# Kernel optimization log

Hardware: AMD Instinct MI355X
Metric: run time of the kernel (lower is better)

The kernel has to match this reference:

```python
import jax, jax.numpy as jnp
import numpy as np

N_NODES = 100000
N_EDGES = 300000
N_GRAPHS = 4096
EMB = 256
L = 5
EPS = 1e-5


def setup_inputs() -> dict:
    key = jax.random.key(0)
    ks = jax.random.split(key, 16)
    x = jax.random.normal(ks[0], (N_NODES, 40), dtype=jnp.float32)
    edge_index = jax.random.randint(ks[1], (2, N_EDGES), 0, N_NODES, dtype=jnp.int32)
    edge_attr = jax.random.normal(ks[2], (N_EDGES, 10), dtype=jnp.float32)
    batch = jnp.sort(jax.random.randint(ks[3], (N_NODES,), 0, N_GRAPHS, dtype=jnp.int32))
    s = lambda fan: 1.0 / np.sqrt(fan)
    params = {
        "x_emb_W": jax.random.normal(ks[4], (EMB, 40), jnp.float32) * np.sqrt(2.0 / 40),
        "x_emb_b": jnp.zeros((EMB,), jnp.float32),
        "e_emb_W": jax.random.normal(ks[5], (EMB, 10), jnp.float32) * np.sqrt(2.0 / 10),
        "e_emb_b": jnp.zeros((EMB,), jnp.float32),
        "gcn_W": jax.random.normal(ks[6], (L, EMB, EMB), jnp.float32) * s(EMB),
        "gcn_b": jax.random.normal(ks[7], (L, EMB), jnp.float32) * s(EMB),
        "root_emb": jax.random.normal(ks[8], (L, EMB), jnp.float32),
        "bn_gamma": jnp.ones((L, EMB), jnp.float32),
        "bn_beta": jnp.zeros((L, EMB), jnp.float32),
        "p1_W": jax.random.normal(ks[9], (EMB // 2, EMB), jnp.float32) * s(EMB),
        "p1_b": jnp.zeros((EMB // 2,), jnp.float32),
        "p2_W": jax.random.normal(ks[10], (EMB // 2, EMB // 2), jnp.float32) * s(EMB // 2),
        "p2_b": jnp.zeros((EMB // 2,), jnp.float32),
        "p3_W": jax.random.normal(ks[11], (1, EMB // 2), jnp.float32) * s(EMB // 2),
        "p3_b": jnp.zeros((1,), jnp.float32),
    }
    return dict(x=x, edge_index=edge_index, edge_attr=edge_attr, batch=batch, **params)


def _gcn_conv(h, row, col, ea, W, b, root):
    # h: [N, D] node feats; ea: [E, D] edge feats
    hx = h @ W.T + b
    deg = jax.ops.segment_sum(jnp.ones_like(row, dtype=hx.dtype), row, num_segments=N_NODES) + 1.0
    dinv = deg ** -0.5
    norm = dinv[row] * dinv[col]                      # [E]
    msg = norm[:, None] * jax.nn.relu(hx[row] + ea)   # gather + relu + scale
    agg = jax.ops.segment_sum(msg, col, num_segments=N_NODES)  # scatter-add to targets
    return agg + jax.nn.relu(hx + root) / deg[:, None]


def _batchnorm(h, gamma, beta):
    mean = jnp.mean(h, axis=0)
    var = jnp.var(h, axis=0)
    return (h - mean) * jax.lax.rsqrt(var + EPS) * gamma + beta


def reference(x, edge_index, edge_attr, batch,
              x_emb_W, x_emb_b, e_emb_W, e_emb_b,
              gcn_W, gcn_b, root_emb, bn_gamma, bn_beta,
              p1_W, p1_b, p2_W, p2_b, p3_W, p3_b):
    row, col = edge_index[0], edge_index[1]
    h = x @ x_emb_W.T + x_emb_b
    ea = edge_attr @ e_emb_W.T + e_emb_b
    for l in range(L):
        h_in = h
        h = _gcn_conv(h, row, col, ea, gcn_W[l], gcn_b[l], root_emb[l])
        h = _batchnorm(h_in + h, bn_gamma[l], bn_beta[l])
        if l != L - 1:
            h = jax.nn.relu(h)
        # dropout is identity in eval mode
    # global mean pool over graphs
    sums = jax.ops.segment_sum(h, batch, num_segments=N_GRAPHS)
    cnts = jax.ops.segment_sum(jnp.ones((h.shape[0],), h.dtype), batch, num_segments=N_GRAPHS)
    g = sums / jnp.maximum(cnts, 1.0)[:, None]
    # prediction head: Lin-ReLU-Lin-ReLU-Lin
    g = jax.nn.relu(g @ p1_W.T + p1_b)
    g = jax.nn.relu(g @ p2_W.T + p2_b)
    return g @ p3_W.T + p3_b
```

## Files before the change

### kernel.cpp

```cpp
#include <hip/hip_runtime.h>
#include <hip/hip_bf16.h>

#define NN 100000
#define NE 300000
#define NG 4096
#define EMB 256
#define NLAYERS 5

typedef unsigned short u16;
typedef unsigned int u32;

typedef short bf16x8 __attribute__((ext_vector_type(8)));
typedef float f32x4 __attribute__((ext_vector_type(4)));

__device__ __forceinline__ float b2f(u16 u){
    union { float f; u32 i; } v; v.i = ((u32)u) << 16; return v.f;
}
__device__ __forceinline__ u16 f2b(float f){
    __hip_bfloat16 h = __float2bfloat16(f);
    union { __hip_bfloat16 h; u16 u; } v; v.h = h; return v.u;
}

#define XNB 32
__global__ __launch_bounds__(256) void embed_x(const float* __restrict__ x,
        const float* __restrict__ W, const float* __restrict__ b,
        u16* __restrict__ t)
{
    __shared__ float sW[256][41];
    __shared__ float sx[XNB][40];
    int tid = threadIdx.x;
    for (int i = tid; i < 256*40; i += 256) sW[i/40][i%40] = W[i];
    int n0 = blockIdx.x * XNB;
    for (int i = tid; i < XNB*40; i += 256) {
        int j = i/40, k = i%40;
        sx[j][k] = x[(size_t)(n0+j)*40 + k];
    }
    __syncthreads();
    float bb = b[tid];
    for (int j = 0; j < XNB; ++j) {
        float a = bb;
        #pragma unroll
        for (int k = 0; k < 40; ++k) a = fmaf(sW[tid][k], sx[j][k], a);
        t[(size_t)(n0+j)*EMB + tid] = f2b(a);
    }
}

__global__ void wconv(const float* __restrict__ W, u16* __restrict__ Wb, int n)
{
    int i = blockIdx.x*256 + threadIdx.x;
    if (i < n) Wb[i] = f2b(W[i]);
}

__global__ void ewt_kernel(const float* __restrict__ eW, float* __restrict__ eWt)
{
    int i = blockIdx.x*256 + threadIdx.x;
    if (i < 2560) { int f = i/10, k = i%10; eWt[k*256 + f] = eW[i]; }
}

__global__ void hist_kernel(const int* __restrict__ row, const int* __restrict__ col,
        int* __restrict__ rcnt, int* __restrict__ ccnt, int E)
{
    int e = blockIdx.x*256 + threadIdx.x;
    if (e < E) {
        atomicAdd(&rcnt[row[e]], 1);
        atomicAdd(&ccnt[col[e]], 1);
    }
}

__global__ void deg_fin(const int* __restrict__ rcnt, float* __restrict__ dinv,
                        float* __restrict__ invdg, int N)
{
    int n = blockIdx.x*256 + threadIdx.x;
    if (n < N) {
        float d = (float)rcnt[n] + 1.0f;
        dinv[n]  = rsqrtf(d);
        invdg[n] = 1.0f/d;
    }
}

__global__ void scan1(const int* __restrict__ cnt, int* __restrict__ bsum, int N)
{
    __shared__ int sh[256];
    int t = threadIdx.x, i = blockIdx.x*256 + t;
    sh[t] = (i < N) ? cnt[i] : 0;
    __syncthreads();
    for (int off = 128; off > 0; off >>= 1) {
        if (t < off) sh[t] += sh[t+off];
        __syncthreads();
    }
    if (t == 0) bsum[blockIdx.x] = sh[0];
}

__global__ __launch_bounds__(512) void scan2(const int* __restrict__ bsum,
        int* __restrict__ bbase, int* __restrict__ coff, int nb)
{
    __shared__ int a[512], b[512];
    int t = threadIdx.x;
    a[t] = (t < nb) ? bsum[t] : 0;
    __syncthreads();
    int* src = a; int* dst = b;
    for (int off = 1; off < 512; off <<= 1) {
        dst[t] = (t >= off) ? src[t-off] + src[t] : src[t];
        __syncthreads();
        int* tmp = src; src = dst; dst = tmp;
    }
    bbase[t] = t ? src[t-1] : 0;
    if (t == 0) coff[NN] = NE;
}

__global__ void scan3(const int* __restrict__ cnt, const int* __restrict__ bbase,
        int* __restrict__ coff, int N)
{
    __shared__ int a[256], b[256];
    int t = threadIdx.x, i = blockIdx.x*256 + t;
    a[t] = (i < N) ? cnt[i] : 0;
    __syncthreads();
    int* src = a; int* dst = b;
    for (int off = 1; off < 256; off <<= 1) {
        dst[t] = (t >= off) ? src[t-off] + src[t] : src[t];
        __syncthreads();
        int* tmp = src; src = dst; dst = tmp;
    }
    if (i < N) coff[i] = bbase[blockIdx.x] + (t ? src[t-1] : 0);
}

__global__ void csr_fill(const int* __restrict__ row, const int* __restrict__ col,
        const float* __restrict__ eattr, const int* __restrict__ coff,
        const float* __restrict__ dinv, int* __restrict__ fill,
        int* __restrict__ erow, float* __restrict__ enorm,
        u16* __restrict__ eab, int E)
{
    int e = blockIdx.x*256 + threadIdx.x;
    if (e < E) {
        int c = col[e], r = row[e];
        int p = coff[c] + atomicAdd(&fill[c], 1);
        erow[p]  = r;
        enorm[p] = dinv[r] * dinv[c];
        #pragma unroll
        for (int k = 0; k < 10; ++k) eab[(size_t)p*16 + k] = f2b(eattr[(size_t)e*10 + k]);
        #pragma unroll
        for (int k = 10; k < 16; ++k) eab[(size_t)p*16 + k] = 0;
    }
}

#define BM 128
#define BK 64
__global__ __launch_bounds__(256) void gemm_mfma(const u16* __restrict__ A,
        const u16* __restrict__ Wb, const float* __restrict__ bias,
        const float* __restrict__ bnsc, int doBN,
        u16* __restrict__ C, int M)
{
    __shared__ u16 As[BM*BK];
    __shared__ u16 Bs[BM*BK];
    __shared__ float scS[256], shS[256];
    const int tid  = threadIdx.x;
    if (doBN) { scS[tid] = bnsc[tid]; shS[tid] = bnsc[256+tid]; }
    const int wid  = tid >> 6;
    const int lane = tid & 63;
    const int wr = wid >> 1, wc = wid & 1;
    const int m0 = blockIdx.x * BM;
    const int n0 = blockIdx.y * BM;
    __syncthreads();
    f32x4 acc[4][4] = {};
    for (int k0 = 0; k0 < 256; k0 += BK) {
        #pragma unroll
        for (int i = 0; i < 4; ++i) {
            int L = tid + i*256;
            int rowi = L >> 3, ch = L & 7;
            int sw = ch ^ (rowi & 7);
            int gr = m0 + rowi; gr = gr < M ? gr : M-1;
            uint4 va = *reinterpret_cast<const uint4*>(&A[(size_t)gr*256 + k0 + ch*8]);
            if (doBN) {
                int kk = k0 + ch*8;
                u32 wv[4] = {va.x, va.y, va.z, va.w};
                #pragma unroll
                for (int j = 0; j < 4; ++j) {
                    float lo = b2f((u16)(wv[j] & 0xffffu));
                    float hi = b2f((u16)(wv[j] >> 16));
                    lo = fmaxf(fmaf(lo, scS[kk+2*j],   shS[kk+2*j]),   0.f);
                    hi = fmaxf(fmaf(hi, scS[kk+2*j+1], shS[kk+2*j+1]), 0.f);
                    wv[j] = (u32)f2b(lo) | ((u32)f2b(hi) << 16);
                }
                va.x = wv[0]; va.y = wv[1]; va.z = wv[2]; va.w = wv[3];
            }
            *reinterpret_cast<uint4*>(&As[(rowi*8 + sw)*8]) = va;
            uint4 vb = *reinterpret_cast<const uint4*>(&Wb[(size_t)(n0+rowi)*256 + k0 + ch*8]);
            *reinterpret_cast<uint4*>(&Bs[(rowi*8 + sw)*8]) = vb;
        }
        __syncthreads();
        const int c = lane >> 4;
        const int rl = lane & 15;
        #pragma unroll
        for (int kt = 0; kt < 2; ++kt) {
            bf16x8 af[4], bfr[4];
            #pragma unroll
            for (int f = 0; f < 4; ++f) {
                int ra = wr*64 + f*16 + rl;
                int cha = (kt*4 + c) ^ (ra & 7);
                af[f] = *reinterpret_cast<const bf16x8*>(&As[(ra*8 + cha)*8]);
                int rb = wc*64 + f*16 + rl;
                int chb = (kt*4 + c) ^ (rb & 7);
                bfr[f] = *reinterpret_cast<const bf16x8*>(&Bs[(rb*8 + chb)*8]);
            }
            #pragma unroll
            for (int fm = 0; fm < 4; ++fm)
                #pragma unroll
                for (int fn = 0; fn < 4; ++fn)
                    acc[fm][fn] = __builtin_amdgcn_mfma_f32_16x16x32_bf16(
                        af[fm], bfr[fn], acc[fm][fn], 0, 0, 0);
        }
        __syncthreads();
    }
    const int cn = lane & 15, rq = lane >> 4;
    #pragma unroll
    for (int fn = 0; fn < 4; ++fn) {
        int n = n0 + wc*64 + fn*16 + cn;
        float bb = bias[n];
        #pragma unroll
        for (int fm = 0; fm < 4; ++fm) {
            #pragma unroll
            for (int r = 0; r < 4; ++r) {
                int m = m0 + wr*64 + fm*16 + rq*4 + r;
                if (m < M) C[(size_t)m*256 + n] = f2b(acc[fm][fn][r] + bb);
            }
        }
    }
}

#define GFB 4
#define NGROUPS (NN/GFB)
__global__ __launch_bounds__(256) void gather_combine(const int* __restrict__ erow,
        const float* __restrict__ enorm, const u16* __restrict__ eab,
        const int* __restrict__ coff,
        const float* __restrict__ eWt, const float* __restrict__ ebv,
        const u16* __restrict__ hx, const float* __restrict__ rootv,
        const float* __restrict__ invdg, const float* __restrict__ bnscPrev,
        int doBN, u16* __restrict__ t, float* __restrict__ stats, int N)
{
    __shared__ float red[4][512];
    const int wid = threadIdx.x >> 6, lane = threadIdx.x & 63;
    const int f4 = lane*4;
    float w[4][10], bb[4];
    #pragma unroll
    for (int k = 0; k < 10; ++k) {
        float4 wv = *reinterpret_cast<const float4*>(&eWt[k*256 + f4]);
        w[0][k] = wv.x; w[1][k] = wv.y; w[2][k] = wv.z; w[3][k] = wv.w;
    }
    { float4 bv = *reinterpret_cast<const float4*>(&ebv[f4]);
      bb[0]=bv.x; bb[1]=bv.y; bb[2]=bv.z; bb[3]=bv.w; }
    float4 root = *reinterpret_cast<const float4*>(&rootv[f4]);
    float sc[4] = {1,1,1,1}, sh[4] = {0,0,0,0};
    if (doBN) {
        float4 s = *reinterpret_cast<const float4*>(&bnscPrev[f4]);
        float4 b = *reinterpret_cast<const float4*>(&bnscPrev[256+f4]);
        sc[0]=s.x; sc[1]=s.y; sc[2]=s.z; sc[3]=s.w;
        sh[0]=b.x; sh[1]=b.y; sh[2]=b.z; sh[3]=b.w;
    }
    float sacc[4] = {0,0,0,0}, s2acc[4] = {0,0,0,0};

    for (int g = blockIdx.x*4 + wid; g < NGROUPS; g += gridDim.x*4) {
        const int nb = g*GFB;
        int c1 = coff[nb+1], c2 = coff[nb+2], c3 = coff[nb+3], c4 = coff[nb+4];
        int s = coff[nb], e = c4;
        int jn = 0, cend = c1;
        float acc[4] = {0,0,0,0};

        #define FLUSH() do {                                                   \
            int n_ = nb + jn;                                                  \
            size_t idx_ = (size_t)n_*EMB + f4;                                 \
            uint2 hv_ = *reinterpret_cast<const uint2*>(&t[idx_]);             \
            uint2 xv_ = *reinterpret_cast<const uint2*>(&hx[idx_]);            \
            float id_ = invdg[n_];                                             \
            float hh_[4] = { b2f((u16)(hv_.x&0xffffu)), b2f((u16)(hv_.x>>16)), \
                             b2f((u16)(hv_.y&0xffffu)), b2f((u16)(hv_.y>>16)) };\
            float xx_[4] = { b2f((u16)(xv_.x&0xffffu)), b2f((u16)(xv_.x>>16)), \
                             b2f((u16)(xv_.y&0xffffu)), b2f((u16)(xv_.y>>16)) };\
            float rt_[4] = { root.x, root.y, root.z, root.w };                 \
            u16 ov_[4];                                                        \
            _Pragma("unroll")                                                  \
            for (int jj = 0; jj < 4; ++jj) {                                   \
                float hin_ = hh_[jj];                                          \
                if (doBN) hin_ = fmaxf(fmaf(hin_, sc[jj], sh[jj]), 0.f);       \
                float rv_ = xx_[jj] + rt_[jj];                                 \
                rv_ = rv_ > 0.f ? rv_ : 0.f;                                   \
                float tv_ = hin_ + acc[jj] + rv_*id_;                          \
                ov_[jj] = f2b(tv_);                                            \
                sacc[jj] += tv_; s2acc[jj] += tv_*tv_;                         \
                acc[jj] = 0.f;                                                 \
            }                                                                  \
            uint2 o_; o_.x = (u32)ov_[0] | ((u32)ov_[1]<<16);                  \
            o_.y = (u32)ov_[2] | ((u32)ov_[3]<<16);                            \
            *reinterpret_cast<uint2*>(&t[idx_]) = o_;                          \
            ++jn; cend = (jn==1) ? c2 : (jn==2) ? c3 : c4;                     \
        } while(0)

        #define CONSUME(nm, hvv, alo, ahi) do {                                \
            float hf_[4] = { b2f((u16)((hvv).x&0xffffu)), b2f((u16)((hvv).x>>16)),\
                             b2f((u16)((hvv).y&0xffffu)), b2f((u16)((hvv).y>>16)) };\
            float at_[10];                                                     \
            at_[0]=b2f((u16)((alo).x&0xffffu)); at_[1]=b2f((u16)((alo).x>>16));\
            at_[2]=b2f((u16)((alo).y&0xffffu)); at_[3]=b2f((u16)((alo).y>>16));\
            at_[4]=b2f((u16)((alo).z&0xffffu)); at_[5]=b2f((u16)((alo).z>>16));\
            at_[6]=b2f((u16)((alo).w&0xffffu)); at_[7]=b2f((u16)((alo).w>>16));\
            at_[8]=b2f((u16)((ahi).x&0xffffu)); at_[9]=b2f((u16)((ahi).x>>16));\
            _Pragma("unroll")                                                  \
            for (int jj = 0; jj < 4; ++jj) {                                   \
                float ea_ = bb[jj];                                            \
                _Pragma("unroll")                                              \
                for (int k = 0; k < 10; ++k) ea_ = fmaf(at_[k], w[jj][k], ea_);\
                float v_ = hf_[jj] + ea_;                                      \
                acc[jj] += v_ > 0.f ? v_*(nm) : 0.f;                           \
            }                                                                  \
        } while(0)

        int p = s;
        for (; p + 4 <= e; p += 4) {
            int r0 = erow[p], r1 = erow[p+1], r2 = erow[p+2], r3 = erow[p+3];
            float n0 = enorm[p], n1 = enorm[p+1], n2 = enorm[p+2], n3 = enorm[p+3];
            uint2 h0 = *reinterpret_cast<const uint2*>(&hx[(size_t)r0*EMB + f4]);
            uint2 h1 = *reinterpret_cast<const uint2*>(&hx[(size_t)r1*EMB + f4]);
            uint2 h2 = *reinterpret_cast<const uint2*>(&hx[(size_t)r2*EMB + f4]);
            uint2 h3 = *reinterpret_cast<const uint2*>(&hx[(size_t)r3*EMB + f4]);
            uint4 a0l = *reinterpret_cast<const uint4*>(&eab[(size_t)(p+0)*16]);
            uint4 a0h = *reinterpret_cast<const uint4*>(&eab[(size_t)(p+0)*16+8]);
            uint4 a1l = *reinterpret_cast<const uint4*>(&eab[(size_t)(p+1)*16]);
            uint4 a1h = *reinterpret_cast<const uint4*>(&eab[(size_t)(p+1)*16+8]);
            uint4 a2l = *reinterpret_cast<const uint4*>(&eab[(size_t)(p+2)*16]);
            uint4 a2h = *reinterpret_cast<const uint4*>(&eab[(size_t)(p+2)*16+8]);
            uint4 a3l = *reinterpret_cast<const uint4*>(&eab[(size_t)(p+3)*16]);
            uint4 a3h = *reinterpret_cast<const uint4*>(&eab[(size_t)(p+3)*16+8]);
            while (p+0 >= cend) FLUSH();
            CONSUME(n0, h0, a0l, a0h);
            while (p+1 >= cend) FLUSH();
            CONSUME(n1, h1, a1l, a1h);
            while (p+2 >= cend) FLUSH();
            CONSUME(n2, h2, a2l, a2h);
            while (p+3 >= cend) FLUSH();
            CONSUME(n3, h3, a3l, a3h);
        }
        for (; p < e; ++p) {
            int r0 = erow[p];
            float n0 = enorm[p];
            uint2 h0 = *reinterpret_cast<const uint2*>(&hx[(size_t)r0*EMB + f4]);
            uint4 a0l = *reinterpret_cast<const uint4*>(&eab[(size_t)p*16]);
            uint4 a0h = *reinterpret_cast<const uint4*>(&eab[(size_t)p*16+8]);
            while (p >= cend) FLUSH();
            CONSUME(n0, h0, a0l, a0h);
        }
        while (jn < GFB) FLUSH();
        #undef FLUSH
        #undef CONSUME
    }

    #pragma unroll
    for (int j = 0; j < 4; ++j) {
        red[wid][f4+j]     = sacc[j];
        red[wid][256+f4+j] = s2acc[j];
    }
    __syncthreads();
    int tt = threadIdx.x;
    float a0 = red[0][tt] + red[1][tt] + red[2][tt] + red[3][tt];
    float a1 = red[0][256+tt] + red[1][256+tt] + red[2][256+tt] + red[3][256+tt];
    atomicAdd(&stats[tt], a0);
    atomicAdd(&stats[256+tt], a1);
}

__global__ void bn_finalize(const float* __restrict__ stats,
        const float* __restrict__ gamma, const float* __restrict__ beta,
        float* __restrict__ sc, int N)
{
    int f = threadIdx.x;
    float inv = 1.0f / (float)N;
    float mean = stats[f] * inv;
    float var  = stats[256+f] * inv - mean*mean;
    float is = rsqrtf(var + 1e-5f);
    float scale = gamma[f] * is;
    sc[f] = scale;
    sc[256+f] = fmaf(-mean, scale, beta[f]);
}

__global__ __launch_bounds__(256) void pool_kernel(const u16* __restrict__ t,
        const int* __restrict__ batch, const float* __restrict__ bnsc4,
        float* __restrict__ psum, float* __restrict__ pcnt, int N)
{
    int f = threadIdx.x;
    float sc = bnsc4[f], shb = bnsc4[256+f];
    int n0 = blockIdx.x * 256;
    int n1 = min(n0 + 256, N);
    int cur = batch[n0];
    float acc = 0.f;
    int cnt = 0;
    for (int n = n0; n < n1; ++n) {
        int g = batch[n];
        if (g != cur) {
            atomicAdd(&psum[(size_t)cur*EMB + f], acc);
            if (f == 0) atomicAdd(&pcnt[cur], (float)cnt);
            acc = 0.f; cnt = 0; cur = g;
        }
        acc += fmaf(b2f(t[(size_t)n*EMB + f]), sc, shb);
        ++cnt;
    }
    atomicAdd(&psum[(size_t)cur*EMB + f], acc);
    if (f == 0) atomicAdd(&pcnt[cur], (float)cnt);
}

__global__ __launch_bounds__(128) void head_kernel(const float* __restrict__ psum,
        const float* __restrict__ pcnt,
        const float* __restrict__ p1W, const float* __restrict__ p1b,
        const float* __restrict__ p2W, const float* __restrict__ p2b,
        const float* __restrict__ p3W, const float* __restrict__ p3b,
        float* __restrict__ out)
{
    __shared__ float gs[256];
    __shared__ float h1[128];
    __shared__ float h2[128];
    __shared__ float red[2];
    int g = blockIdx.x, t = threadIdx.x;
    float invc = 1.0f / fmaxf(pcnt[g], 1.0f);
    gs[t]       = psum[(size_t)g*EMB + t] * invc;
    gs[t + 128] = psum[(size_t)g*EMB + 128 + t] * invc;
    __syncthreads();
    float a = p1b[t];
    for (int k = 0; k < 256; ++k) a = fmaf(p1W[(size_t)t*256 + k], gs[k], a);
    h1[t] = fmaxf(a, 0.f);
    __syncthreads();
    float b = p2b[t];
    for (int k = 0; k < 128; ++k) b = fmaf(p2W[(size_t)t*128 + k], h1[k], b);
    h2[t] = fmaxf(b, 0.f);
    __syncthreads();
    float r = p3W[t] * h2[t];
    for (int off = 32; off > 0; off >>= 1) r += __shfl_down(r, off);
    if ((t & 63) == 0) red[t >> 6] = r;
    __syncthreads();
    if (t == 0) out[g] = red[0] + red[1] + p3b[0];
}

extern "C" void kernel_launch(void* const* d_in, const int* in_sizes, int n_in,
                              void* d_out, int out_size, void* d_ws, size_t ws_size,
                              hipStream_t stream)
{
    const float* x     = (const float*)d_in[0];
    const int*   eidx  = (const int*)d_in[1];
    const float* eattr = (const float*)d_in[2];
    const int*   batch = (const int*)d_in[3];
    const float* xW    = (const float*)d_in[4];
    const float* xb    = (const float*)d_in[5];
    const float* eW    = (const float*)d_in[6];
    const float* eb    = (const float*)d_in[7];
    const float* gcnW  = (const float*)d_in[8];
    const float* gcnb  = (const float*)d_in[9];
    const float* rootE = (const float*)d_in[10];
    const float* bng   = (const float*)d_in[11];
    const float* bnb   = (const float*)d_in[12];
    const float* p1W   = (const float*)d_in[13];
    const float* p1b   = (const float*)d_in[14];
    const float* p2W   = (const float*)d_in[15];
    const float* p2b   = (const float*)d_in[16];
    const float* p3W   = (const float*)d_in[17];
    const float* p3b   = (const float*)d_in[18];
    float* out = (float*)d_out;

    const int* row = eidx;
    const int* col = eidx + NE;

    const size_t HSZ = (size_t)NN * EMB;
    const int NWB = 5*EMB*EMB;

    char* p = (char*)d_ws;
    u16* t   = (u16*)p;            p += HSZ*2;
    u16* hx  = (u16*)p;            p += HSZ*2;
    u16* Wb  = (u16*)p;            p += (size_t)NWB*2;
    float* eWt = (float*)p;        p += 2560*4;
    char* zbase = p;
    int* rcnt   = (int*)p;         p += (size_t)NN*4;
    int* ccnt   = (int*)p;         p += (size_t)NN*4;
    int* fill   = (int*)p;         p += (size_t)NN*4;
    float* stats= (float*)p;       p += (size_t)NLAYERS*512*4;
    float* psum = (float*)p;       p += (size_t)NG*EMB*4;
    float* pcnt = (float*)p;       p += (size_t)NG*4;
    size_t zbytes = (size_t)(p - zbase);
    float* dinv = (float*)p;       p += (size_t)NN*4;
    float* invdg= (float*)p;       p += (size_t)NN*4;
    float* bnscA= (float*)p;       p += (size_t)NLAYERS*512*4;
    int* coff   = (int*)p;         p += (size_t)(NN+1)*4;
    int* bsum   = (int*)p;         p += 512*4;
    int* bbase  = (int*)p;         p += 512*4;
    int* erow   = (int*)p;         p += (size_t)NE*4;
    float* enorm= (float*)p;       p += (size_t)NE*4;
    u16* eab    = (u16*)p;         p += (size_t)NE*16*2;
    size_t NEED = (size_t)(p - (char*)d_ws);
    if (ws_size < NEED) return;

    hipMemsetAsync(zbase, 0, zbytes, stream);

    const int NBS = (NN + 255)/256;

    embed_x<<<NN/XNB, 256, 0, stream>>>(x, xW, xb, t);
    wconv<<<(NWB+255)/256, 256, 0, stream>>>(gcnW, Wb, NWB);
    ewt_kernel<<<10, 256, 0, stream>>>(eW, eWt);
    hist_kernel<<<(NE+255)/256, 256, 0, stream>>>(row, col, rcnt, ccnt, NE);
    deg_fin<<<NBS, 256, 0, stream>>>(rcnt, dinv, invdg, NN);
    scan1<<<NBS, 256, 0, stream>>>(ccnt, bsum, NN);
    scan2<<<1, 512, 0, stream>>>(bsum, bbase, coff, NBS);
    scan3<<<NBS, 256, 0, stream>>>(ccnt, bbase, coff, NN);
    csr_fill<<<(NE+255)/256, 256, 0, stream>>>(row, col, eattr, coff, dinv, fill,
                                               erow, enorm, eab, NE);

    for (int l = 0; l < NLAYERS; ++l) {
        const u16*   Wl = Wb + (size_t)l*EMB*EMB;
        const float* bl = gcnb + (size_t)l*EMB;
        const float* rl = rootE + (size_t)l*EMB;
        const float* scPrev = bnscA + (size_t)(l > 0 ? l-1 : 0)*512;
        int doBN = (l > 0) ? 1 : 0;
        dim3 ggrid((NN + BM - 1)/BM, EMB/BM);
        gemm_mfma<<<ggrid, 256, 0, stream>>>(t, Wl, bl, scPrev, doBN, hx, NN);
        gather_combine<<<1536, 256, 0, stream>>>(erow, enorm, eab, coff, eWt, eb,
                hx, rl, invdg, scPrev, doBN, t, stats + l*512, NN);
        bn_finalize<<<1, 256, 0, stream>>>(stats + l*512, bng + (size_t)l*EMB,
                                           bnb + (size_t)l*EMB, bnscA + (size_t)l*512, NN);
    }

    pool_kernel<<<NBS, 256, 0, stream>>>(t, batch, bnscA + (size_t)(NLAYERS-1)*512,
                                         psum, pcnt, NN);
    head_kernel<<<NG, 128, 0, stream>>>(psum, pcnt, p1W, p1b, p2W, p2b, p3W, p3b, out);
}
```

Baseline: 1.007 ms.

## Widen GCN GEMM tile to full N, vectorize pooling, move head to MFMA GEMMs

```diff
diff --git a/kernel.cpp b/kernel.cpp
--- a/kernel.cpp
+++ b/kernel.cpp
@@ -143,29 +143,26 @@
     }
 }
 
-#define BM 128
-#define BK 64
-__global__ __launch_bounds__(256) void gemm_mfma(const u16* __restrict__ A,
+__global__ __launch_bounds__(512) void gemm_mfma(const u16* __restrict__ A,
         const u16* __restrict__ Wb, const float* __restrict__ bias,
         const float* __restrict__ bnsc, int doBN,
         u16* __restrict__ C, int M)
 {
-    __shared__ u16 As[BM*BK];
-    __shared__ u16 Bs[BM*BK];
+    __shared__ u16 As[128*64];
+    __shared__ u16 Bs[256*64];
     __shared__ float scS[256], shS[256];
-    const int tid  = threadIdx.x;
-    if (doBN) { scS[tid] = bnsc[tid]; shS[tid] = bnsc[256+tid]; }
+    const int tid = threadIdx.x;
+    if (doBN && tid < 256) { scS[tid] = bnsc[tid]; shS[tid] = bnsc[256+tid]; }
     const int wid  = tid >> 6;
     const int lane = tid & 63;
-    const int wr = wid >> 1, wc = wid & 1;
-    const int m0 = blockIdx.x * BM;
-    const int n0 = blockIdx.y * BM;
+    const int wm = wid >> 2, wn = wid & 3;
+    const int m0 = blockIdx.x * 128;
     __syncthreads();
     f32x4 acc[4][4] = {};
-    for (int k0 = 0; k0 < 256; k0 += BK) {
-        #pragma unroll
-        for (int i = 0; i < 4; ++i) {
-            int L = tid + i*256;
+    for (int k0 = 0; k0 < 256; k0 += 64) {
+        #pragma unroll
+        for (int i = 0; i < 2; ++i) {
+            int L = tid + i*512;
             int rowi = L >> 3, ch = L & 7;
             int sw = ch ^ (rowi & 7);
             int gr = m0 + rowi; gr = gr < M ? gr : M-1;
@@ -184,7 +181,13 @@
                 va.x = wv[0]; va.y = wv[1]; va.z = wv[2]; va.w = wv[3];
             }
             *reinterpret_cast<uint4*>(&As[(rowi*8 + sw)*8]) = va;
-            uint4 vb = *reinterpret_cast<const uint4*>(&Wb[(size_t)(n0+rowi)*256 + k0 + ch*8]);
+        }
+        #pragma unroll
+        for (int i = 0; i < 4; ++i) {
+            int L = tid + i*512;
+            int rowi = L >> 3, ch = L & 7;
+            int sw = ch ^ (rowi & 7);
+            uint4 vb = *reinterpret_cast<const uint4*>(&Wb[(size_t)rowi*256 + k0 + ch*8]);
             *reinterpret_cast<uint4*>(&Bs[(rowi*8 + sw)*8]) = vb;
         }
         __syncthreads();
@@ -195,10 +198,10 @@
             bf16x8 af[4], bfr[4];
             #pragma unroll
             for (int f = 0; f < 4; ++f) {
-                int ra = wr*64 + f*16 + rl;
+                int ra = wm*64 + f*16 + rl;
                 int cha = (kt*4 + c) ^ (ra & 7);
                 af[f] = *reinterpret_cast<const bf16x8*>(&As[(ra*8 + cha)*8]);
-                int rb = wc*64 + f*16 + rl;
+                int rb = wn*64 + f*16 + rl;
                 int chb = (kt*4 + c) ^ (rb & 7);
                 bfr[f] = *reinterpret_cast<const bf16x8*>(&Bs[(rb*8 + chb)*8]);
             }
@@ -214,13 +217,13 @@
     const int cn = lane & 15, rq = lane >> 4;
     #pragma unroll
     for (int fn = 0; fn < 4; ++fn) {
-        int n = n0 + wc*64 + fn*16 + cn;
+        int n = wn*64 + fn*16 + cn;
         float bb = bias[n];
         #pragma unroll
         for (int fm = 0; fm < 4; ++fm) {
             #pragma unroll
             for (int r = 0; r < 4; ++r) {
-                int m = m0 + wr*64 + fm*16 + rq*4 + r;
+                int m = m0 + wm*64 + fm*16 + rq*4 + r;
                 if (m < M) C[(size_t)m*256 + n] = f2b(acc[fm][fn][r] + bb);
             }
         }
@@ -383,56 +386,134 @@
         const int* __restrict__ batch, const float* __restrict__ bnsc4,
         float* __restrict__ psum, float* __restrict__ pcnt, int N)
 {
-    int f = threadIdx.x;
-    float sc = bnsc4[f], shb = bnsc4[256+f];
+    int tid = threadIdx.x;
+    int half = tid >> 7;
+    int pp = tid & 127;
+    const u32* t32 = (const u32*)t;
+    float sc0 = bnsc4[2*pp],     sc1 = bnsc4[2*pp+1];
+    float sh0 = bnsc4[256+2*pp], sh1 = bnsc4[256+2*pp+1];
     int n0 = blockIdx.x * 256;
     int n1 = min(n0 + 256, N);
-    int cur = batch[n0];
-    float acc = 0.f;
+    int start = n0 + half;
+    if (start >= n1) return;
+    int cur = batch[start];
+    float a0 = 0.f, a1 = 0.f;
     int cnt = 0;
-    for (int n = n0; n < n1; ++n) {
-        int g = batch[n];
-        if (g != cur) {
-            atomicAdd(&psum[(size_t)cur*EMB + f], acc);
-            if (f == 0) atomicAdd(&pcnt[cur], (float)cnt);
-            acc = 0.f; cnt = 0; cur = g;
-        }
-        acc += fmaf(b2f(t[(size_t)n*EMB + f]), sc, shb);
+    for (int n = start; n < n1; n += 2) {
+        int gb = batch[n];
+        if (gb != cur) {
+            atomicAdd(&psum[(size_t)cur*EMB + 2*pp],   a0);
+            atomicAdd(&psum[(size_t)cur*EMB + 2*pp+1], a1);
+            if (pp == 0) atomicAdd(&pcnt[cur], (float)cnt);
+            a0 = a1 = 0.f; cnt = 0; cur = gb;
+        }
+        u32 v = t32[(size_t)n*128 + pp];
+        a0 += fmaf(b2f((u16)(v & 0xffffu)), sc0, sh0);
+        a1 += fmaf(b2f((u16)(v >> 16)),     sc1, sh1);
         ++cnt;
     }
-    atomicAdd(&psum[(size_t)cur*EMB + f], acc);
-    if (f == 0) atomicAdd(&pcnt[cur], (float)cnt);
-}
-
-__global__ __launch_bounds__(128) void head_kernel(const float* __restrict__ psum,
-        const float* __restrict__ pcnt,
-        const float* __restrict__ p1W, const float* __restrict__ p1b,
-        const float* __restrict__ p2W, const float* __restrict__ p2b,
+    atomicAdd(&psum[(size_t)cur*EMB + 2*pp],   a0);
+    atomicAdd(&psum[(size_t)cur*EMB + 2*pp+1], a1);
+    if (pp == 0) atomicAdd(&pcnt[cur], (float)cnt);
+}
+
+__global__ void pool2g(const float* __restrict__ psum, const float* __restrict__ pcnt,
+        u16* __restrict__ gbf)
+{
+    int i = blockIdx.x*256 + threadIdx.x;
+    if (i < NG*128) {
+        int g = i >> 7, p2 = (i & 127)*2;
+        float invc = 1.0f / fmaxf(pcnt[g], 1.0f);
+        u32 pk = (u32)f2b(psum[(size_t)g*EMB + p2] * invc)
+               | ((u32)f2b(psum[(size_t)g*EMB + p2 + 1] * invc) << 16);
+        ((u32*)gbf)[i] = pk;
+    }
+}
+
+__global__ __launch_bounds__(256) void gemm_head(const u16* __restrict__ A,
+        const u16* __restrict__ W, const float* __restrict__ bias,
+        u16* __restrict__ C, int M, int K)
+{
+    __shared__ u16 As[128*64];
+    __shared__ u16 Bs[128*64];
+    const int tid  = threadIdx.x;
+    const int wid  = tid >> 6;
+    const int lane = tid & 63;
+    const int wr = wid >> 1, wc = wid & 1;
+    const int m0 = blockIdx.x * 128;
+    f32x4 acc[4][4] = {};
+    for (int k0 = 0; k0 < K; k0 += 64) {
+        #pragma unroll
+        for (int i = 0; i < 4; ++i) {
+            int L = tid + i*256;
+            int rowi = L >> 3, ch = L & 7;
+            int sw = ch ^ (rowi & 7);
+            int gr = m0 + rowi; gr = gr < M ? gr : M-1;
+            uint4 va = *reinterpret_cast<const uint4*>(&A[(size_t)gr*K + k0 + ch*8]);
+            *reinterpret_cast<uint4*>(&As[(rowi*8 + sw)*8]) = va;
+            uint4 vb = *reinterpret_cast<const uint4*>(&W[(size_t)rowi*K + k0 + ch*8]);
+            *reinterpret_cast<uint4*>(&Bs[(rowi*8 + sw)*8]) = vb;
+        }
+        __syncthreads();
+        const int c = lane >> 4;
+        const int rl = lane & 15;
+        #pragma unroll
+        for (int kt = 0; kt < 2; ++kt) {
+            bf16x8 af[4], bfr[4];
+            #pragma unroll
+            for (int f = 0; f < 4; ++f) {
+                int ra = wr*64 + f*16 + rl;
+                int cha = (kt*4 + c) ^ (ra & 7);
+                af[f] = *reinterpret_cast<const bf16x8*>(&As[(ra*8 + cha)*8]);
+                int rb = wc*64 + f*16 + rl;
+                int chb = (kt*4 + c) ^ (rb & 7);
+                bfr[f] = *reinterpret_cast<const bf16x8*>(&Bs[(rb*8 + chb)*8]);
+            }
+            #pragma unroll
+            for (int fm = 0; fm < 4; ++fm)
+                #pragma unroll
+                for (int fn = 0; fn < 4; ++fn)
+                    acc[fm][fn] = __builtin_amdgcn_mfma_f32_16x16x32_bf16(
+                        af[fm], bfr[fn], acc[fm][fn], 0, 0, 0);
+        }
+        __syncthreads();
+    }
+    const int cn = lane & 15, rq = lane >> 4;
+    #pragma unroll
+    for (int fn = 0; fn < 4; ++fn) {
+        int n = wc*64 + fn*16 + cn;
+        float bb = bias[n];
+        #pragma unroll
+        for (int fm = 0; fm < 4; ++fm) {
+            #pragma unroll
+            for (int r = 0; r < 4; ++r) {
+                int m = m0 + wr*64 + fm*16 + rq*4 + r;
+                if (m < M) C[(size_t)m*128 + n] = f2b(fmaxf(acc[fm][fn][r] + bb, 0.f));
+            }
+        }
+    }
+}
+
+__global__ __launch_bounds__(256) void head_final(const u16* __restrict__ h2,
         const float* __restrict__ p3W, const float* __restrict__ p3b,
-        float* __restrict__ out)
-{
-    __shared__ float gs[256];
-    __shared__ float h1[128];
-    __shared__ float h2[128];
-    __shared__ float red[2];
-    int g = blockIdx.x, t = threadIdx.x;
-    float invc = 1.0f / fmaxf(pcnt[g], 1.0f);
-    gs[t]       = psum[(size_t)g*EMB + t] * invc;
-    gs[t + 128] = psum[(size_t)g*EMB + 128 + t] * invc;
-    __syncthreads();
-    float a = p1b[t];
-    for (int k = 0; k < 256; ++k) a = fmaf(p1W[(size_t)t*256 + k], gs[k], a);
-    h1[t] = fmaxf(a, 0.f);
-    __syncthreads();
-    float b = p2b[t];
-    for (int k = 0; k < 128; ++k) b = fmaf(p2W[(size_t)t*128 + k], h1[k], b);
-    h2[t] = fmaxf(b, 0.f);
-    __syncthreads();
-    float r = p3W[t] * h2[t];
-    for (int off = 32; off > 0; off >>= 1) r += __shfl_down(r, off);
-    if ((t & 63) == 0) red[t >> 6] = r;
-    __syncthreads();
-    if (t == 0) out[g] = red[0] + red[1] + p3b[0];
+        float* __restrict__ out, int G)
+{
+    int tid = blockIdx.x*256 + threadIdx.x;
+    int g = tid >> 4, sub = tid & 15;
+    if (g >= G) return;
+    uint4 v = *reinterpret_cast<const uint4*>(&h2[(size_t)g*128 + sub*8]);
+    u32 wv[4] = {v.x, v.y, v.z, v.w};
+    float s = 0.f;
+    #pragma unroll
+    for (int j = 0; j < 4; ++j) {
+        s = fmaf(b2f((u16)(wv[j] & 0xffffu)), p3W[sub*8 + 2*j],   s);
+        s = fmaf(b2f((u16)(wv[j] >> 16)),     p3W[sub*8 + 2*j+1], s);
+    }
+    s += __shfl_down(s, 8, 16);
+    s += __shfl_down(s, 4, 16);
+    s += __shfl_down(s, 2, 16);
+    s += __shfl_down(s, 1, 16);
+    if (sub == 0) out[g] = s + p3b[0];
 }
 
 extern "C" void kernel_launch(void* const* d_in, const int* in_sizes, int n_in,
@@ -488,6 +569,11 @@
     int* erow   = (int*)p;         p += (size_t)NE*4;
     float* enorm= (float*)p;       p += (size_t)NE*4;
     u16* eab    = (u16*)p;         p += (size_t)NE*16*2;
+    u16* gbf    = (u16*)p;         p += (size_t)NG*EMB*2;
+    u16* h1b    = (u16*)p;         p += (size_t)NG*128*2;
+    u16* h2b    = (u16*)p;         p += (size_t)NG*128*2;
+    u16* Wh1    = (u16*)p;         p += (size_t)128*256*2;
+    u16* Wh2    = (u16*)p;         p += (size_t)128*128*2;
     size_t NEED = (size_t)(p - (char*)d_ws);
     if (ws_size < NEED) return;
 
@@ -497,6 +583,8 @@
 
     embed_x<<<NN/XNB, 256, 0, stream>>>(x, xW, xb, t);
     wconv<<<(NWB+255)/256, 256, 0, stream>>>(gcnW, Wb, NWB);
+    wconv<<<(128*256+255)/256, 256, 0, stream>>>(p1W, Wh1, 128*256);
+    wconv<<<(128*128+255)/256, 256, 0, stream>>>(p2W, Wh2, 128*128);
     ewt_kernel<<<10, 256, 0, stream>>>(eW, eWt);
     hist_kernel<<<(NE+255)/256, 256, 0, stream>>>(row, col, rcnt, ccnt, NE);
     deg_fin<<<NBS, 256, 0, stream>>>(rcnt, dinv, invdg, NN);
@@ -512,8 +600,7 @@
         const float* rl = rootE + (size_t)l*EMB;
         const float* scPrev = bnscA + (size_t)(l > 0 ? l-1 : 0)*512;
         int doBN = (l > 0) ? 1 : 0;
-        dim3 ggrid((NN + BM - 1)/BM, EMB/BM);
-        gemm_mfma<<<ggrid, 256, 0, stream>>>(t, Wl, bl, scPrev, doBN, hx, NN);
+        gemm_mfma<<<(NN+127)/128, 512, 0, stream>>>(t, Wl, bl, scPrev, doBN, hx, NN);
         gather_combine<<<1536, 256, 0, stream>>>(erow, enorm, eab, coff, eWt, eb,
                 hx, rl, invdg, scPrev, doBN, t, stats + l*512, NN);
         bn_finalize<<<1, 256, 0, stream>>>(stats + l*512, bng + (size_t)l*EMB,
@@ -522,5 +609,8 @@
 
     pool_kernel<<<NBS, 256, 0, stream>>>(t, batch, bnscA + (size_t)(NLAYERS-1)*512,
                                          psum, pcnt, NN);
-    head_kernel<<<NG, 128, 0, stream>>>(psum, pcnt, p1W, p1b, p2W, p2b, p3W, p3b, out);
-}
+    pool2g<<<(NG*128+255)/256, 256, 0, stream>>>(psum, pcnt, gbf);
+    gemm_head<<<NG/128, 256, 0, stream>>>(gbf, Wh1, p1b, h1b, NG, 256);
+    gemm_head<<<NG/128, 256, 0, stream>>>(h1b, Wh2, p2b, h2b, NG, 128);
+    head_final<<<(NG*16+255)/256, 256, 0, stream>>>(h2b, p3W, p3b, out, NG);
+}
```

Measured after the change: 970.1 us. -3.6%, faster.
